# Kernel tuning notes

Hardware: AMD Instinct MI355X
Metric: run time of the kernel (lower is better)

## Reference

```python
import jax, jax.numpy as jnp
import numpy as np

B, S, K = 2, 256, 2          # batch, seq, banks_selected (top-k)
IN, OUT, NB = 512, 512, 16   # in_features, out_features, num_banks


def setup_inputs() -> dict:
    key = jax.random.key(0)
    k1, k2, k3, k4 = jax.random.split(key, 4)
    bound = 1.0 / np.sqrt(IN)  # nn.Linear default init range
    tensor = jax.random.normal(k1, (B, S, K, IN), dtype=jnp.float32)
    bank_selections = jax.random.randint(k2, (B, S, K), 0, NB)
    # stacked nn.Linear params: weight (num_banks, out, in), bias (num_banks, out)
    weight = jax.random.uniform(k3, (NB, OUT, IN), dtype=jnp.float32, minval=-bound, maxval=bound)
    bias = jax.random.uniform(k4, (NB, OUT), dtype=jnp.float32, minval=-bound, maxval=bound)
    return {"tensor": tensor, "bank_selections": bank_selections, "weight": weight, "bias": bias}


def reference(tensor, bank_selections, weight, bias):
    # Gather per-selection weights/bias, exactly as extract_weights/extract_bias.
    w_sel = weight[bank_selections]  # (B, S, K, OUT, IN) -- the large expanded intermediate
    b_sel = bias[bank_selections]    # (B, S, K, OUT)
    # Per-selection linear: out[..., k, :] = x[..., k, :] @ W[sel[..., k]].T + b[sel[..., k]]
    return jnp.einsum('bski,bskoi->bsko', tensor, w_sel) + b_sel
```

## Files before the change

kernel.cpp:

```cpp
#include <hip/hip_runtime.h>

#define NB   16
#define INF  512
#define OUTF 512
#define MAXT 80

typedef __attribute__((ext_vector_type(8))) short bf16x8;
typedef __attribute__((ext_vector_type(4))) float f32x4;

static __device__ __forceinline__ ushort f2bf(float f) {
    unsigned u = __float_as_uint(f);
    u += 0x7FFFu + ((u >> 16) & 1u);
    return (ushort)(u >> 16);
}

#define HDR_INTS (MAXT)

__global__ __launch_bounds__(256) void prep_kernel(
    const float* __restrict__ x, const int* __restrict__ sel,
    const float* __restrict__ W,
    int* __restrict__ tiles, int* __restrict__ lists,
    ushort* __restrict__ xb, ushort* __restrict__ Wb, int nrows)
{
    int t = threadIdx.x;
    if (blockIdx.x == 0) {
        __shared__ int cnt[NB];
        if (t < NB) cnt[t] = 0;
        __syncthreads();
        for (int r = t; r < nrows; r += 256) {
            int b = sel[r];
            int pos = atomicAdd(&cnt[b], 1);
            lists[b * nrows + pos] = r;
        }
        __syncthreads();
        if (t == 0) {
            if (cnt[0] == 0) lists[0] = 0;
            int nt = 0;
            for (int b = 0; b < NB; ++b) {
                int c = cnt[b];
                for (int r0 = 0; r0 < c; r0 += 16) {
                    int m = c - r0; if (m > 16) m = 16;
                    tiles[nt++] = (b << 20) | (r0 << 8) | m;
                }
            }
            for (; nt < MAXT; ++nt) tiles[nt] = 0;
        }
        return;
    }
    const int nvw = NB * OUTF * INF / 4;
    const int nvx = (nrows * INF) / 4;
    int gid = (blockIdx.x - 1) * 256 + t;
    int stride = (gridDim.x - 1) * 256;
    const float4* Wf = (const float4*)W;
    const float4* xf = (const float4*)x;
    ushort4* Wo = (ushort4*)Wb;
    ushort4* xo = (ushort4*)xb;
    for (int i = gid; i < nvw + nvx; i += stride) {
        if (i < nvw) {
            float4 v = Wf[i];
            ushort4 o;
            o.x = f2bf(v.x); o.y = f2bf(v.y); o.z = f2bf(v.z); o.w = f2bf(v.w);
            Wo[i] = o;
        } else {
            int j = i - nvw;
            float4 v = xf[j];
            ushort4 o;
            o.x = f2bf(v.x); o.y = f2bf(v.y); o.z = f2bf(v.z); o.w = f2bf(v.w);
            xo[j] = o;
        }
    }
}

__global__ __launch_bounds__(256) void mfma_gemm(
    const ushort* __restrict__ xb, const ushort* __restrict__ Wb,
    const float* __restrict__ bias, const int* __restrict__ tiles,
    const int* __restrict__ lists, float* __restrict__ out, int nrows_total)
{
    int tb = tiles[blockIdx.y];
    int mrows = tb & 0xff;
    if (mrows == 0) return;
    int bank = tb >> 20;
    int row0 = (tb >> 8) & 0xfff;

    int lane = threadIdx.x & 63;
    int wave = threadIdx.x >> 6;
    int ln = lane & 15;
    int q  = lane >> 4;

    int o = blockIdx.x * 64 + wave * 16 + ln;
    int rg = lists[bank * nrows_total + row0 + (ln < mrows ? ln : 0)];
    float bv = bias[bank * OUTF + o];

    const ushort* ap = xb + (size_t)rg * INF + q * 8;
    const ushort* bp = Wb + ((size_t)bank * OUTF + o) * INF + q * 8;

    f32x4 acc0 = {0.f, 0.f, 0.f, 0.f};
    f32x4 acc1 = {0.f, 0.f, 0.f, 0.f};
#pragma unroll
    for (int i = 0; i < 8; ++i) {
        bf16x8 a0 = *(const bf16x8*)(ap + (2 * i) * 32);
        bf16x8 b0 = *(const bf16x8*)(bp + (2 * i) * 32);
        bf16x8 a1 = *(const bf16x8*)(ap + (2 * i + 1) * 32);
        bf16x8 b1 = *(const bf16x8*)(bp + (2 * i + 1) * 32);
        acc0 = __builtin_amdgcn_mfma_f32_16x16x32_bf16(a0, b0, acc0, 0, 0, 0);
        acc1 = __builtin_amdgcn_mfma_f32_16x16x32_bf16(a1, b1, acc1, 0, 0, 0);
    }

#pragma unroll
    for (int r = 0; r < 4; ++r) {
        int m = q * 4 + r;
        int rowg = __shfl(rg, m, 16);
        if (m < mrows)
            out[(size_t)rowg * OUTF + o] = acc0[r] + acc1[r] + bv;
    }
}

extern "C" void kernel_launch(void* const* d_in, const int* in_sizes, int n_in,
                              void* d_out, int out_size, void* d_ws, size_t ws_size,
                              hipStream_t stream) {
    const float* tensor = (const float*)d_in[0];
    const int*   sel    = (const int*)d_in[1];
    const float* weight = (const float*)d_in[2];
    const float* bias   = (const float*)d_in[3];
    float* out = (float*)d_out;

    int nrows = in_sizes[1];

    int* tiles = (int*)d_ws;
    int* lists = tiles + HDR_INTS;
    size_t int_bytes = (size_t)(HDR_INTS + NB * nrows) * sizeof(int);
    size_t xb_bytes  = (size_t)nrows * INF * sizeof(ushort);
    ushort* xb = (ushort*)((char*)d_ws + int_bytes);
    ushort* Wb = (ushort*)((char*)d_ws + int_bytes + xb_bytes);

    prep_kernel<<<1025, 256, 0, stream>>>(tensor, sel, weight, tiles, lists,
                                          xb, Wb, nrows);
    dim3 grid(OUTF / 64, MAXT, 1);
    mfma_gemm<<<grid, 256, 0, stream>>>(xb, Wb, bias, tiles, lists, out, nrows);
}
```

Baseline: 87.66 us.

## Fuse fp32-to-bf16 conversion into GEMM loads, drop separate prep pass

Removes the global conversion pass that wrote bf16 copies of all weights and inputs to workspace. The GEMM now reads fp32 directly and converts to bf16 in registers before each MFMA, leaving only a tiny bucketing kernel beforehand. This avoids writing and re-reading a full bf16 weight copy, at the cost of doubling the bytes each GEMM tile loads and adding conversion ALU work inside the inner loop.

```diff
diff --git a/kernel.cpp b/kernel.cpp
--- a/kernel.cpp
+++ b/kernel.cpp
@@ -14,65 +14,47 @@
     return (ushort)(u >> 16);
 }
 
-#define HDR_INTS (MAXT)
+static __device__ __forceinline__ bf16x8 cvt8(const float* __restrict__ p) {
+    float4 v0 = *(const float4*)p;
+    float4 v1 = *(const float4*)(p + 4);
+    bf16x8 r;
+    r[0] = (short)f2bf(v0.x); r[1] = (short)f2bf(v0.y);
+    r[2] = (short)f2bf(v0.z); r[3] = (short)f2bf(v0.w);
+    r[4] = (short)f2bf(v1.x); r[5] = (short)f2bf(v1.y);
+    r[6] = (short)f2bf(v1.z); r[7] = (short)f2bf(v1.w);
+    return r;
+}
 
-__global__ __launch_bounds__(256) void prep_kernel(
-    const float* __restrict__ x, const int* __restrict__ sel,
-    const float* __restrict__ W,
-    int* __restrict__ tiles, int* __restrict__ lists,
-    ushort* __restrict__ xb, ushort* __restrict__ Wb, int nrows)
+__global__ __launch_bounds__(256) void bucket_kernel(
+    const int* __restrict__ sel, int* __restrict__ tiles,
+    int* __restrict__ lists, int nrows)
 {
+    __shared__ int cnt[NB];
     int t = threadIdx.x;
-    if (blockIdx.x == 0) {
-        __shared__ int cnt[NB];
-        if (t < NB) cnt[t] = 0;
-        __syncthreads();
-        for (int r = t; r < nrows; r += 256) {
-            int b = sel[r];
-            int pos = atomicAdd(&cnt[b], 1);
-            lists[b * nrows + pos] = r;
+    if (t < NB) cnt[t] = 0;
+    __syncthreads();
+    for (int r = t; r < nrows; r += 256) {
+        int b = sel[r];
+        int pos = atomicAdd(&cnt[b], 1);
+        lists[b * nrows + pos] = r;
+    }
+    __syncthreads();
+    if (t == 0) {
+        if (cnt[0] == 0) lists[0] = 0;
+        int nt = 0;
+        for (int b = 0; b < NB; ++b) {
+            int c = cnt[b];
+            for (int r0 = 0; r0 < c; r0 += 16) {
+                int m = c - r0; if (m > 16) m = 16;
+                tiles[nt++] = (b << 20) | (r0 << 8) | m;
+            }
         }
-        __syncthreads();
-        if (t == 0) {
-            if (cnt[0] == 0) lists[0] = 0;
-            int nt = 0;
-            for (int b = 0; b < NB; ++b) {
-                int c = cnt[b];
-                for (int r0 = 0; r0 < c; r0 += 16) {
-                    int m = c - r0; if (m > 16) m = 16;
-                    tiles[nt++] = (b << 20) | (r0 << 8) | m;
-                }
-            }
-            for (; nt < MAXT; ++nt) tiles[nt] = 0;
-        }
-        return;
-    }
-    const int nvw = NB * OUTF * INF / 4;
-    const int nvx = (nrows * INF) / 4;
-    int gid = (blockIdx.x - 1) * 256 + t;
-    int stride = (gridDim.x - 1) * 256;
-    const float4* Wf = (const float4*)W;
-    const float4* xf = (const float4*)x;
-    ushort4* Wo = (ushort4*)Wb;
-    ushort4* xo = (ushort4*)xb;
-    for (int i = gid; i < nvw + nvx; i += stride) {
-        if (i < nvw) {
-            float4 v = Wf[i];
-            ushort4 o;
-            o.x = f2bf(v.x); o.y = f2bf(v.y); o.z = f2bf(v.z); o.w = f2bf(v.w);
-            Wo[i] = o;
-        } else {
-            int j = i - nvw;
-            float4 v = xf[j];
-            ushort4 o;
-            o.x = f2bf(v.x); o.y = f2bf(v.y); o.z = f2bf(v.z); o.w = f2bf(v.w);
-            xo[j] = o;
-        }
+        for (; nt < MAXT; ++nt) tiles[nt] = 0;
     }
 }
 
 __global__ __launch_bounds__(256) void mfma_gemm(
-    const ushort* __restrict__ xb, const ushort* __restrict__ Wb,
+    const float* __restrict__ x, const float* __restrict__ W,
     const float* __restrict__ bias, const int* __restrict__ tiles,
     const int* __restrict__ lists, float* __restrict__ out, int nrows_total)
 {
@@ -91,19 +73,18 @@
     int rg = lists[bank * nrows_total + row0 + (ln < mrows ? ln : 0)];
     float bv = bias[bank * OUTF + o];
 
-    const ushort* ap = xb + (size_t)rg * INF + q * 8;
-    const ushort* bp = Wb + ((size_t)bank * OUTF + o) * INF + q * 8;
+    const float* ap = x + (size_t)rg * INF + q * 8;
+    const float* bp = W + ((size_t)bank * OUTF + o) * INF + q * 8;
 
-    f32x4 acc0 = {0.f, 0.f, 0.f, 0.f};
-    f32x4 acc1 = {0.f, 0.f, 0.f, 0.f};
-#pragma unroll
-    for (int i = 0; i < 8; ++i) {
-        bf16x8 a0 = *(const bf16x8*)(ap + (2 * i) * 32);
-        bf16x8 b0 = *(const bf16x8*)(bp + (2 * i) * 32);
-        bf16x8 a1 = *(const bf16x8*)(ap + (2 * i + 1) * 32);
-        bf16x8 b1 = *(const bf16x8*)(bp + (2 * i + 1) * 32);
-        acc0 = __builtin_amdgcn_mfma_f32_16x16x32_bf16(a0, b0, acc0, 0, 0, 0);
-        acc1 = __builtin_amdgcn_mfma_f32_16x16x32_bf16(a1, b1, acc1, 0, 0, 0);
+    f32x4 acc[2];
+    acc[0] = (f32x4){0.f, 0.f, 0.f, 0.f};
+    acc[1] = (f32x4){0.f, 0.f, 0.f, 0.f};
+#pragma unroll 4
+    for (int i = 0; i < 16; ++i) {
+        bf16x8 a = cvt8(ap + i * 32);
+        bf16x8 b = cvt8(bp + i * 32);
+        acc[i & 1] = __builtin_amdgcn_mfma_f32_16x16x32_bf16(a, b, acc[i & 1],
+                                                             0, 0, 0);
     }
 
 #pragma unroll
@@ -111,7 +92,7 @@
         int m = q * 4 + r;
         int rowg = __shfl(rg, m, 16);
         if (m < mrows)
-            out[(size_t)rowg * OUTF + o] = acc0[r] + acc1[r] + bv;
+            out[(size_t)rowg * OUTF + o] = acc[0][r] + acc[1][r] + bv;
     }
 }
 
@@ -127,14 +108,10 @@
     int nrows = in_sizes[1];
 
     int* tiles = (int*)d_ws;
-    int* lists = tiles + HDR_INTS;
-    size_t int_bytes = (size_t)(HDR_INTS + NB * nrows) * sizeof(int);
-    size_t xb_bytes  = (size_t)nrows * INF * sizeof(ushort);
-    ushort* xb = (ushort*)((char*)d_ws + int_bytes);
-    ushort* Wb = (ushort*)((char*)d_ws + int_bytes + xb_bytes);
+    int* lists = tiles + MAXT;
 
-    prep_kernel<<<1025, 256, 0, stream>>>(tensor, sel, weight, tiles, lists,
-                                          xb, Wb, nrows);
+    bucket_kernel<<<1, 256, 0, stream>>>(sel, tiles, lists, nrows);
     dim3 grid(OUTF / 64, MAXT, 1);
-    mfma_gemm<<<grid, 256, 0, stream>>>(xb, Wb, bias, tiles, lists, out, nrows);
+    mfma_gemm<<<grid, 256, 0, stream>>>(tensor, weight, bias, tiles, lists, out,
+                                        nrows);
 }
```

Measured after the change: 97.98 us. 11.8% more time.
